# Kernel optimization log

Measured on AMD Instinct MI355X. Metric: run time of the kernel, lower is better.

The kernel has to match this reference:

```python
import jax, jax.numpy as jnp
import numpy as np
from jax import lax

B, P, S, H, F, V, O = 32, 24, 48, 512, 64, 50000, 16
EPS = 1e-5


def _lstm_scan(inputs, Wih, Whh, b):
    # inputs: [T, B, D]; PyTorch gate order i, f, g, o
    def step(carry, xt):
        h, c = carry
        g = xt @ Wih.T + h @ Whh.T + b
        i, f, gg, o = jnp.split(g, 4, axis=-1)
        c = jax.nn.sigmoid(f) * c + jax.nn.sigmoid(i) * jnp.tanh(gg)
        h = jax.nn.sigmoid(o) * jnp.tanh(c)
        return (h, c), h
    b_ = inputs.shape[1]
    h0 = jnp.zeros((b_, Whh.shape[1]), inputs.dtype)
    _, hs = lax.scan(step, (h0, h0), inputs)
    return hs


def setup_inputs() -> dict:
    key = jax.random.key(0)
    ks = jax.random.split(key, 16)
    x = jax.random.randint(ks[0], (B, P, S), 0, V)
    lens = jnp.sort(jax.random.randint(ks[1], (B,), 1, P + 1))[::-1]
    lens = lens.at[0].set(P)  # pack_padded: sorted desc, max len == P
    tok_len = jax.random.randint(ks[2], (B, P), 1, S + 1)
    tok_len = tok_len * (jnp.arange(P)[None, :] < lens[:, None])
    x_mask = jnp.arange(S)[None, None, :] >= tok_len[:, :, None]  # True = pad
    x_feature = jax.random.normal(ks[3], (B, P, S, F), dtype=jnp.float32)
    emb = jax.random.normal(ks[4], (V, H), dtype=jnp.float32) * 0.02
    w_attn = jax.random.normal(ks[5], (H,), dtype=jnp.float32) * 0.02
    b_attn = jnp.zeros((), jnp.float32)
    D = H + F
    s = 1.0 / np.sqrt(H)
    u = lambda k, sh: jax.random.uniform(k, sh, jnp.float32, -s, s)
    Wih_f, Whh_f = u(ks[6], (4 * H, D)), u(ks[7], (4 * H, H))
    bih_f, bhh_f = u(ks[8], (4 * H,)), u(ks[9], (4 * H,))
    Wih_b, Whh_b = u(ks[10], (4 * H, D)), u(ks[11], (4 * H, H))
    bih_b, bhh_b = u(ks[12], (4 * H,)), u(ks[13], (4 * H,))
    Wfc = u(ks[14], (O, 2 * H))
    bfc = jnp.zeros((O,), jnp.float32)
    gamma = jnp.ones((O,), jnp.float32)
    beta = jnp.zeros((O,), jnp.float32)
    return {"x": x, "x_mask": x_mask, "x_feature": x_feature,
            "sentences_len": lens, "clause": 0, "cls": 0,
            "emb": emb, "w_attn": w_attn, "b_attn": b_attn,
            "Wih_f": Wih_f, "Whh_f": Whh_f, "bih_f": bih_f, "bhh_f": bhh_f,
            "Wih_b": Wih_b, "Whh_b": Whh_b, "bih_b": bih_b, "bhh_b": bhh_b,
            "Wfc": Wfc, "bfc": bfc, "gamma": gamma, "beta": beta}


def reference(x, x_mask, x_feature, sentences_len, clause, cls,
              emb, w_attn, b_attn,
              Wih_f, Whh_f, bih_f, bhh_f,
              Wih_b, Whh_b, bih_b, bhh_b,
              Wfc, bfc, gamma, beta):
    # --- per-sentence embed + linear self-attention + masked sum pooling ---
    e = emb[x]                                             # [B,P,S,H]
    scores = jnp.einsum('bpsh,h->bps', e, w_attn) + b_attn  # [B,P,S]
    scores = jnp.where(x_mask, -1e30, scores)
    alpha = jax.nn.softmax(scores, axis=-1)
    alpha = jnp.where(x_mask, 0.0, alpha)                  # zeros empty sents; relu(softmax)=softmax
    valid = (~x_mask).astype(e.dtype)
    weighted = e * alpha[..., None]
    cat = jnp.concatenate([weighted, x_feature], axis=-1) * valid[..., None]
    rep = cat.sum(axis=2)                                  # [B,P,H+F]
    seq = jnp.transpose(rep, (1, 0, 2))                    # time-major [P,B,H+F]

    # --- packed bidirectional LSTM (per-sequence reversal for bwd dir) ---
    t = jnp.arange(P)[:, None]                             # [P,1]
    lens = sentences_len[None, :]                          # [1,B]
    valid_t = (t < lens)                                   # [P,B]
    h_fwd = _lstm_scan(seq, Wih_f, Whh_f, bih_f + bhh_f)
    rev_idx = jnp.clip(lens - 1 - t, 0)                    # [P,B]
    rev_in = jnp.take_along_axis(seq, rev_idx[..., None], axis=0)
    h_bwd_rev = _lstm_scan(rev_in, Wih_b, Whh_b, bih_b + bhh_b)
    h_bwd = jnp.take_along_axis(h_bwd_rev, rev_idx[..., None], axis=0)
    out_seq = jnp.concatenate([h_fwd, h_bwd], axis=-1) * valid_t[..., None]  # pad_packed zeros

    # --- tail: last timestep, fc, train-mode BN, relu, log_softmax(dim=0) ---
    last = out_seq[-1]                                     # [B,2H]
    z = jnp.reshape(last.T, (B, 2 * H))                    # faithful transpose+view quirk
    y = z @ Wfc.T + bfc                                    # [B,O]
    mean = y.mean(axis=0)
    var = y.var(axis=0)                                    # biased, as torch BN normalization
    y = gamma * (y - mean) / jnp.sqrt(var + EPS) + beta
    y = jax.nn.relu(y)
    return jax.nn.log_softmax(y, axis=0)
```

## Files before the change

kernel.cpp:

```cpp
#include <hip/hip_runtime.h>
#include <math.h>

#define BB_ 32
#define PP_ 24
#define SS_ 48
#define HH_ 512
#define FF_ 64
#define DD_ 576
#define G4_ 2048

typedef __attribute__((ext_vector_type(8))) short short8;
typedef __attribute__((ext_vector_type(4))) float f32x4;

__device__ __forceinline__ float sigf(float x) { return 1.f / (1.f + expf(-x)); }

__device__ __forceinline__ unsigned short f2bf(float f) {
    unsigned int u = __float_as_uint(f);
    u += 0x7FFFu + ((u >> 16) & 1u);
    return (unsigned short)(u >> 16);
}

__global__ void __launch_bounds__(256) prep_attn_kernel(
        const int* __restrict__ x, const unsigned int* __restrict__ maskw,
        const float* __restrict__ x_feature, const float* __restrict__ emb,
        const float* __restrict__ w_attn, const float* __restrict__ b_attn,
        const float* __restrict__ Whh, unsigned short* __restrict__ Bf,
        const float* __restrict__ Wih, unsigned short* __restrict__ Wbf,
        float* __restrict__ AfA, int* __restrict__ flags,
        float* __restrict__ seq)
{
    int blk = blockIdx.x, tid = threadIdx.x;
    if (blk < 768) {
        __shared__ float sc_s[SS_], alpha_s[SS_];
        __shared__ int vtok[SS_], vpos[SS_];
        __shared__ int nv_s, s_u8, s_f32;
        __shared__ int idx_s[SS_];
        __shared__ unsigned char msk_s[SS_];
        if (tid == 0) { s_u8 = 0; s_f32 = 0; }
        __syncthreads();
        int u8 = 0, f32 = 0;
        for (int i = tid; i < 9216; i += 256) {
            unsigned int w = maskw[i];
            if (w == 0x3F800000u) f32 = 1;
            else if (w > 1u) u8 = 1;
        }
        if (u8) s_u8 = 1;
        if (f32) s_f32 = 1;
        __syncthreads();
        int mode = s_f32 ? 2 : (s_u8 ? 1 : 0);
        int bp = blk, b = bp / PP_, p = bp % PP_;
        if (tid < SS_) {
            size_t i = (size_t)bp * SS_ + tid;
            idx_s[tid] = x[i];
            unsigned char mv;
            if (mode == 1)      mv = ((const unsigned char*)maskw)[i];
            else if (mode == 2) mv = (((const float*)maskw)[i] != 0.f);
            else                mv = (((const int*)maskw)[i] != 0);
            msk_s[tid] = mv;
        }
        __syncthreads();
        if (tid == 0) {
            int nv = 0;
            for (int s = 0; s < SS_; ++s)
                if (!msk_s[s]) { vtok[nv] = idx_s[s]; vpos[nv] = s; ++nv; }
            nv_s = nv;
        }
        __syncthreads();
        int nv = nv_s;
        int wave = tid >> 6, lane = tid & 63;
        float4 wa0 = ((const float4*)w_attn)[lane];
        float4 wa1 = ((const float4*)w_attn)[64 + lane];
        for (int j = wave; j < nv; j += 4) {
            const float4* er4 = (const float4*)(emb + (size_t)vtok[j] * HH_);
            float4 v0 = er4[lane], v1 = er4[64 + lane];
            float acc = v0.x * wa0.x + v0.y * wa0.y + v0.z * wa0.z + v0.w * wa0.w
                      + v1.x * wa1.x + v1.y * wa1.y + v1.z * wa1.z + v1.w * wa1.w;
            #pragma unroll
            for (int off = 32; off > 0; off >>= 1) acc += __shfl_down(acc, off, 64);
            if (lane == 0) sc_s[j] = acc + b_attn[0];
        }
        __syncthreads();
        if (tid == 0) {
            float m = -3.4e38f;
            for (int j = 0; j < nv; ++j) if (sc_s[j] > m) m = sc_s[j];
            float sum = 0.f;
            for (int j = 0; j < nv; ++j) { float a = expf(sc_s[j] - m); alpha_s[j] = a; sum += a; }
            float inv = (nv > 0) ? (1.f / sum) : 0.f;
            for (int j = 0; j < nv; ++j) alpha_s[j] *= inv;
        }
        __syncthreads();
        float acc0 = 0.f, acc1 = 0.f;
        for (int j = 0; j < nv; ++j) {
            float a = alpha_s[j];
            const float* er = emb + (size_t)vtok[j] * HH_;
            acc0 += a * er[tid];
            acc1 += a * er[tid + 256];
        }
        float* orow = seq + ((size_t)p * BB_ + b) * DD_;
        orow[tid] = acc0;
        orow[tid + 256] = acc1;
        if (tid < FF_) {
            float accF = 0.f;
            for (int j = 0; j < nv; ++j)
                accF += x_feature[((size_t)bp * SS_ + vpos[j]) * FF_ + tid];
            orow[HH_ + tid] = accF;
        }
    } else if (blk < 1280) {
        int idx = (blk - 768) * 256 + tid;
        int lane = idx & 63;
        int ks = (idx >> 6) & 15;
        int ti = (idx >> 10) & 1;
        int nb = idx >> 11;
        int c = lane & 15, q = lane >> 4;
        int nrow = (ti * 2 + (c >> 3)) * HH_ + nb * 8 + (c & 7);
        int k0 = ks * 32 + q * 8;
        const float* src = Whh + (size_t)nrow * HH_ + k0;
        unsigned int w0 = (unsigned int)f2bf(src[0]) | ((unsigned int)f2bf(src[1]) << 16);
        unsigned int w1 = (unsigned int)f2bf(src[2]) | ((unsigned int)f2bf(src[3]) << 16);
        unsigned int w2 = (unsigned int)f2bf(src[4]) | ((unsigned int)f2bf(src[5]) << 16);
        unsigned int w3 = (unsigned int)f2bf(src[6]) | ((unsigned int)f2bf(src[7]) << 16);
        *(uint4*)(Bf + (size_t)idx * 8) = make_uint4(w0, w1, w2, w3);
    } else if (blk < 2432) {
        int i = (blk - 1280) * 256 + tid;
        float4 v = ((const float4*)Wih)[i];
        ushort4 o;
        o.x = f2bf(v.x); o.y = f2bf(v.y); o.z = f2bf(v.z); o.w = f2bf(v.w);
        ((ushort4*)Wbf)[i] = o;
    } else if (blk < 2464) {
        int idx = (blk - 2432) * 256 + tid;
        if (idx < 8192) AfA[idx] = 0.f;
    } else {
        if (tid < 64) flags[tid] = 0;
    }
}

__global__ void __launch_bounds__(256) in_gates_mfma_kernel(
        const float* __restrict__ A,
        const unsigned short* __restrict__ Wbf,
        const float* __restrict__ bih,
        const float* __restrict__ bhh,
        float* __restrict__ Cout)
{
    int tid = threadIdx.x, lane = tid & 63, w = tid >> 6;
    int m0 = blockIdx.y * 16;
    int nb = blockIdx.x * 128 + w * 32;
    int c = lane & 15, q = lane >> 4;
    const float* Ap = A + (size_t)(m0 + c) * DD_ + q * 8;
    const unsigned short* Bp0 = Wbf + (size_t)(nb + c) * DD_ + q * 8;
    const unsigned short* Bp1 = Bp0 + 16 * DD_;
    f32x4 acc0 = {0.f, 0.f, 0.f, 0.f}, acc1 = {0.f, 0.f, 0.f, 0.f};
    for (int k = 0; k < DD_; k += 32) {
        float4 alo = *(const float4*)(Ap + k);
        float4 ahi = *(const float4*)(Ap + k + 4);
        short8 a;
        a[0] = (short)f2bf(alo.x); a[1] = (short)f2bf(alo.y);
        a[2] = (short)f2bf(alo.z); a[3] = (short)f2bf(alo.w);
        a[4] = (short)f2bf(ahi.x); a[5] = (short)f2bf(ahi.y);
        a[6] = (short)f2bf(ahi.z); a[7] = (short)f2bf(ahi.w);
        short8 b0 = *(const short8*)(Bp0 + k);
        short8 b1 = *(const short8*)(Bp1 + k);
        acc0 = __builtin_amdgcn_mfma_f32_16x16x32_bf16(a, b0, acc0, 0, 0, 0);
        acc1 = __builtin_amdgcn_mfma_f32_16x16x32_bf16(a, b1, acc1, 0, 0, 0);
    }
    #pragma unroll
    for (int r = 0; r < 4; ++r) {
        int m = m0 + q * 4 + r;
        int n0 = nb + c, n1 = nb + 16 + c;
        Cout[(size_t)m * G4_ + n0] = acc0[r] + bih[n0] + bhh[n0];
        Cout[(size_t)m * G4_ + n1] = acc1[r] + bih[n1] + bhh[n1];
    }
}

__global__ void __launch_bounds__(256) lstm_bwd_kernel(
        unsigned short* __restrict__ AfA, unsigned short* __restrict__ AfB,
        float* __restrict__ hbuf, const float* __restrict__ Ain,
        const unsigned short* __restrict__ Bfrag, int* __restrict__ flags,
        const float* __restrict__ seq, const int* __restrict__ lens,
        const float* __restrict__ Wih_b, const float* __restrict__ bih_b,
        const float* __restrict__ bhh_b, float* __restrict__ hbw)
{
    __shared__ float smem[19040];
    int tid = threadIdx.x;
    if (blockIdx.x < 64) {
        float* gl = smem;
        unsigned short* hstage = (unsigned short*)(smem + 1056);
        int lane = tid & 63, wv = tid >> 6;
        int mt = wv & 1, ti = wv >> 1;
        int nb = blockIdx.x;
        const short8* Bp = (const short8*)Bfrag + (((size_t)nb * 2 + ti) * 16) * 64 + lane;
        short8 bfr[16];
        #pragma unroll
        for (int ks = 0; ks < 16; ++ks) bfr[ks] = Bp[ks * 64];
        int c = lane & 15, q = lane >> 4;
        int g = ti * 2 + (c >> 3), ul = c & 7;
        int b2 = tid >> 3, u2 = tid & 7;
        int ug = nb * 8 + u2;
        float creg = 0.f;
        for (int t = 0; t < PP_; ++t) {
            const unsigned short* Af = (t & 1) ? AfB : AfA;
            unsigned short* An       = (t & 1) ? AfA : AfB;
            const float* Ain_t = Ain + (size_t)t * BB_ * G4_;
            float ainv[4];
            #pragma unroll
            for (int r = 0; r < 4; ++r)
                ainv[r] = Ain_t[(size_t)(mt * 16 + q * 4 + r) * G4_ + g * HH_ + nb * 8 + ul];
            const unsigned long long* Ap64 =
                (const unsigned long long*)Af + ((size_t)(mt * 16) * 64 + lane) * 2;
            short8 a[16];
            #pragma unroll
            for (int ks = 0; ks < 16; ++ks) {
                unsigned long long lo = __hip_atomic_load(Ap64 + (size_t)ks * 128,
                        __ATOMIC_RELAXED, __HIP_MEMORY_SCOPE_AGENT);
                unsigned long long hi = __hip_atomic_load(Ap64 + (size_t)ks * 128 + 1,
                        __ATOMIC_RELAXED, __HIP_MEMORY_SCOPE_AGENT);
                union { unsigned long long u[2]; short8 s; } cv;
                cv.u[0] = lo; cv.u[1] = hi;
                a[ks] = cv.s;
            }
            f32x4 acA = {0.f, 0.f, 0.f, 0.f}, acB = {0.f, 0.f, 0.f, 0.f};
            #pragma unroll
            for (int ks = 0; ks < 16; ks += 2) {
                acA = __builtin_amdgcn_mfma_f32_16x16x32_bf16(a[ks],     bfr[ks],     acA, 0, 0, 0);
                acB = __builtin_amdgcn_mfma_f32_16x16x32_bf16(a[ks + 1], bfr[ks + 1], acB, 0, 0, 0);
            }
            #pragma unroll
            for (int r = 0; r < 4; ++r) {
                float v = acA[r] + acB[r] + ainv[r];
                v = (g == 2) ? tanhf(v) : sigf(v);
                gl[(g * 8 + ul) * 33 + (mt * 16 + q * 4 + r)] = v;
            }
            __syncthreads();
            float iv = gl[(0  + u2) * 33 + b2];
            float fv = gl[(8  + u2) * 33 + b2];
            float gv = gl[(16 + u2) * 33 + b2];
            float ov = gl[(24 + u2) * 33 + b2];
            creg = fv * creg + iv * gv;
            float h = ov * tanhf(creg);
            if (t == PP_ - 1) {
                hbuf[(size_t)b2 * HH_ + ug] = h;
            } else {
                hstage[tid] = f2bf(h);
                __syncthreads();
                if (tid < 64) {
                    int b2s = tid >> 1, hf2 = tid & 1;
                    const unsigned short* hp = &hstage[b2s * 8 + hf2 * 4];
                    unsigned long long v = (unsigned long long)hp[0]
                                         | ((unsigned long long)hp[1] << 16)
                                         | ((unsigned long long)hp[2] << 32)
                                         | ((unsigned long long)hp[3] << 48);
                    size_t ub = ((((size_t)(b2s >> 4)) * 16 + (nb >> 2)) * 64
                                 + ((b2s & 15) + 16 * (nb & 3))) * 8 + hf2 * 4;
                    __hip_atomic_store((unsigned long long*)(An + ub), v,
                                       __ATOMIC_RELAXED, __HIP_MEMORY_SCOPE_AGENT);
                }
                __syncthreads();
                if (tid == 0)
                    __hip_atomic_store(&flags[nb], t + 1,
                                       __ATOMIC_RELAXED, __HIP_MEMORY_SCOPE_AGENT);
                if (tid < 64) {
                    int target = t + 1;
                    while (true) {
                        int v = __hip_atomic_load(&flags[tid],
                                __ATOMIC_RELAXED, __HIP_MEMORY_SCOPE_AGENT);
                        if (__all(v >= target)) break;
                        __builtin_amdgcn_s_sleep(1);
                    }
                }
                __syncthreads();
            }
        }
    } else {
        float* xsT = smem;
        int* pl = (int*)(smem + 19008);
        int blk2 = blockIdx.x - 64;
        if (tid < BB_) pl[tid] = lens[tid] - 1;
        __syncthreads();
        for (int idx = tid; idx < BB_ * DD_; idx += 256) {
            int b2 = idx / DD_;
            int k = idx - b2 * DD_;
            xsT[k * 33 + b2] = seq[((size_t)pl[b2] * BB_ + b2) * DD_ + k];
        }
        __syncthreads();
        int b = tid & 31, ul = tid >> 5;
        int u = blk2 * 8 + ul;
        const float* wi = Wih_b + (size_t)u * DD_;
        const float* wg = Wih_b + (size_t)(2 * HH_ + u) * DD_;
        const float* wo = Wih_b + (size_t)(3 * HH_ + u) * DD_;
        float gi = 0.f, gg = 0.f, go = 0.f;
        #pragma unroll 4
        for (int k = 0; k < DD_; k += 4) {
            float4 w1 = *(const float4*)(wi + k);
            float4 w2 = *(const float4*)(wg + k);
            float4 w3 = *(const float4*)(wo + k);
            float x0 = xsT[(k + 0) * 33 + b];
            float x1 = xsT[(k + 1) * 33 + b];
            float x2 = xsT[(k + 2) * 33 + b];
            float x3 = xsT[(k + 3) * 33 + b];
            gi += w1.x * x0 + w1.y * x1 + w1.z * x2 + w1.w * x3;
            gg += w2.x * x0 + w2.y * x1 + w2.z * x2 + w2.w * x3;
            go += w3.x * x0 + w3.y * x1 + w3.z * x2 + w3.w * x3;
        }
        gi += bih_b[u] + bhh_b[u];
        gg += bih_b[2 * HH_ + u] + bhh_b[2 * HH_ + u];
        go += bih_b[3 * HH_ + u] + bhh_b[3 * HH_ + u];
        float cc = sigf(gi) * tanhf(gg);
        hbw[(size_t)b * HH_ + u] = sigf(go) * tanhf(cc);
    }
}

__global__ void __launch_bounds__(1024) head_fused_kernel(
        const float* __restrict__ hf, const float* __restrict__ hbwd,
        const int* __restrict__ lens,
        const float* __restrict__ Wfc, const float* __restrict__ bfc,
        const float* __restrict__ gamma, const float* __restrict__ beta,
        float* __restrict__ out)
{
    __shared__ float tileL[32 * 1024];
    __shared__ float lmask[BB_];
    __shared__ float part[1024];
    __shared__ float ys[16][33];
    __shared__ float cstat[16];
    int tid = threadIdx.x;
    if (tid < BB_) lmask[tid] = (lens[tid] == PP_) ? 1.f : 0.f;
    __syncthreads();
    for (int j = tid; j < 32 * 1024; j += 1024) {
        int bb = j >> 10, col = j & 1023;
        float v = (col < HH_) ? hf[(size_t)bb * HH_ + col]
                              : hbwd[(size_t)bb * HH_ + col - HH_];
        tileL[j] = v * lmask[bb];
    }
    __syncthreads();
    int outi = tid & 511, half = tid >> 9;
    int i = outi >> 4, o = outi & 15;
    const float* wrow = Wfc + (size_t)o * 1024;
    float acc = 0.f;
    for (int q = 0; q < 32; ++q) {
        int j = i * 32 + q;
        #pragma unroll
        for (int bb2 = 0; bb2 < 16; ++bb2) {
            int bb = half * 16 + bb2;
            acc += tileL[bb * 1024 + j] * wrow[q * 32 + bb];
        }
    }
    part[tid] = acc;
    __syncthreads();
    if (tid < 512) ys[o][i] = part[tid] + part[tid + 512] + bfc[o];
    __syncthreads();
    if (tid < 16) {
        float mean = 0.f;
        for (int ii = 0; ii < 32; ++ii) mean += ys[tid][ii];
        mean *= (1.f / 32.f);
        float var = 0.f;
        for (int ii = 0; ii < 32; ++ii) { float d = ys[tid][ii] - mean; var += d * d; }
        var *= (1.f / 32.f);
        float inv = 1.f / sqrtf(var + 1e-5f);
        float gmm = gamma[tid], bt = beta[tid];
        float mx = -3.4e38f;
        for (int ii = 0; ii < 32; ++ii) {
            float v = gmm * (ys[tid][ii] - mean) * inv + bt;
            v = fmaxf(v, 0.f);
            ys[tid][ii] = v;
            mx = fmaxf(mx, v);
        }
        float s = 0.f;
        for (int ii = 0; ii < 32; ++ii) s += expf(ys[tid][ii] - mx);
        cstat[tid] = mx + logf(s);
    }
    __syncthreads();
    if (tid < 512) out[tid] = ys[o][i] - cstat[o];
}

extern "C" void kernel_launch(void* const* d_in, const int* in_sizes, int n_in,
                              void* d_out, int out_size, void* d_ws, size_t ws_size,
                              hipStream_t stream) {
    const int* x            = (const int*)d_in[0];
    const void* xm          = d_in[1];
    const float* x_feature  = (const float*)d_in[2];
    const int* lens         = (const int*)d_in[3];
    const float* emb    = (const float*)d_in[6];
    const float* w_attn = (const float*)d_in[7];
    const float* b_attn = (const float*)d_in[8];
    const float* Wih_f  = (const float*)d_in[9];
    const float* Whh_f  = (const float*)d_in[10];
    const float* bih_f  = (const float*)d_in[11];
    const float* bhh_f  = (const float*)d_in[12];
    const float* Wih_b  = (const float*)d_in[13];
    const float* bih_b  = (const float*)d_in[15];
    const float* bhh_b  = (const float*)d_in[16];
    const float* Wfc    = (const float*)d_in[17];
    const float* bfc    = (const float*)d_in[18];
    const float* gamma  = (const float*)d_in[19];
    const float* beta   = (const float*)d_in[20];

    float* ws    = (float*)d_ws;
    float* seq   = ws;
    float* Ain   = seq + (size_t)PP_ * BB_ * DD_;
    float* hb    = Ain + (size_t)PP_ * BB_ * G4_;
    float* hbuf  = hb + (size_t)BB_ * HH_;
    float* AfA   = hbuf + (size_t)BB_ * HH_;
    float* AfB   = AfA + 8192;
    float* Bfrag = AfB + 8192;
    float* Wbf   = Bfrag + 524288;
    int*  flags  = (int*)(Wbf + 589824);

    float* outp = (float*)d_out;

    prep_attn_kernel<<<dim3(2465), dim3(256), 0, stream>>>(
        x, (const unsigned int*)xm, x_feature, emb, w_attn, b_attn,
        Whh_f, (unsigned short*)Bfrag, Wih_f, (unsigned short*)Wbf,
        AfA, flags, seq);
    in_gates_mfma_kernel<<<dim3(16, 48), dim3(256), 0, stream>>>(
        seq, (const unsigned short*)Wbf, bih_f, bhh_f, Ain);
    lstm_bwd_kernel<<<dim3(128), dim3(256), 0, stream>>>(
        (unsigned short*)AfA, (unsigned short*)AfB, hbuf, Ain,
        (const unsigned short*)Bfrag, flags,
        seq, lens, Wih_b, bih_b, bhh_b, hb);
    head_fused_kernel<<<dim3(1), dim3(1024), 0, stream>>>(
        hbuf, hb, lens, Wfc, bfc, gamma, beta, outp);
}
```

Baseline: 440.7 us.

## Consolidate forward LSTM recurrence onto 16 blocks with 32 units each

The persistent forward-LSTM recurrence now runs on 16 workgroups instead of 64. Each workgroup owns 32 hidden units, and each wave keeps 4 gate tiles of bf16 Whh fragments in registers. The Whh fragment layout is reordered to match, the Ain input is folded into the MFMA accumulator init, and each thread writes its packed h values straight to global memory without a shared-memory staging pass. The aim is to cut the cost of the per-timestep cross-block flag barrier (fewer participants) and remove one __syncthreads per step. In exchange each block does four times the MFMA work per step, and register pressure rises, which may cause spills.

```diff
diff --git a/kernel.cpp b/kernel.cpp
--- a/kernel.cpp
+++ b/kernel.cpp
@@ -109,10 +109,11 @@
         int idx = (blk - 768) * 256 + tid;
         int lane = idx & 63;
         int ks = (idx >> 6) & 15;
-        int ti = (idx >> 10) & 1;
-        int nb = idx >> 11;
+        int j = (idx >> 10) & 7;
+        int nb = idx >> 13;
         int c = lane & 15, q = lane >> 4;
-        int nrow = (ti * 2 + (c >> 3)) * HH_ + nb * 8 + (c & 7);
+        int g = j >> 1, tt = j & 1;
+        int nrow = g * HH_ + nb * 32 + tt * 16 + c;
         int k0 = ks * 32 + q * 8;
         const float* src = Whh + (size_t)nrow * HH_ + k0;
         unsigned int w0 = (unsigned int)f2bf(src[0]) | ((unsigned int)f2bf(src[1]) << 16);
@@ -171,7 +172,7 @@
     }
 }
 
-__global__ void __launch_bounds__(256) lstm_bwd_kernel(
+__global__ void __launch_bounds__(256, 1) lstm_bwd_kernel(
         unsigned short* __restrict__ AfA, unsigned short* __restrict__ AfB,
         float* __restrict__ hbuf, const float* __restrict__ Ain,
         const unsigned short* __restrict__ Bfrag, int* __restrict__ flags,
@@ -181,31 +182,41 @@
 {
     __shared__ float smem[19040];
     int tid = threadIdx.x;
-    if (blockIdx.x < 64) {
+    if (blockIdx.x < 16) {
         float* gl = smem;
-        unsigned short* hstage = (unsigned short*)(smem + 1056);
         int lane = tid & 63, wv = tid >> 6;
-        int mt = wv & 1, ti = wv >> 1;
+        int mt = wv & 1, h2 = wv >> 1;
         int nb = blockIdx.x;
-        const short8* Bp = (const short8*)Bfrag + (((size_t)nb * 2 + ti) * 16) * 64 + lane;
-        short8 bfr[16];
-        #pragma unroll
-        for (int ks = 0; ks < 16; ++ks) bfr[ks] = Bp[ks * 64];
         int c = lane & 15, q = lane >> 4;
-        int g = ti * 2 + (c >> 3), ul = c & 7;
-        int b2 = tid >> 3, u2 = tid & 7;
-        int ug = nb * 8 + u2;
-        float creg = 0.f;
+        short8 bfr[4][16];
+        {
+            const short8* Bp = (const short8*)Bfrag;
+            #pragma unroll
+            for (int jj = 0; jj < 4; ++jj) {
+                const short8* bp = Bp + ((size_t)(nb * 8 + h2 * 4 + jj) * 16) * 64 + lane;
+                #pragma unroll
+                for (int ks = 0; ks < 16; ++ks) bfr[jj][ks] = bp[(size_t)ks * 64];
+            }
+        }
+        int mt_e = tid >> 7, le = (tid >> 1) & 63, half = tid & 1;
+        int be = mt_e * 16 + (le & 15);
+        int ue0 = (le >> 4) * 8 + half * 4;
+        float creg[4] = {0.f, 0.f, 0.f, 0.f};
         for (int t = 0; t < PP_; ++t) {
             const unsigned short* Af = (t & 1) ? AfB : AfA;
             unsigned short* An       = (t & 1) ? AfA : AfB;
             const float* Ain_t = Ain + (size_t)t * BB_ * G4_;
-            float ainv[4];
-            #pragma unroll
-            for (int r = 0; r < 4; ++r)
-                ainv[r] = Ain_t[(size_t)(mt * 16 + q * 4 + r) * G4_ + g * HH_ + nb * 8 + ul];
+            f32x4 acc[4];
+            #pragma unroll
+            for (int jj = 0; jj < 4; ++jj) {
+                int g = h2 * 2 + (jj >> 1), tt = jj & 1;
+                int n = g * HH_ + nb * 32 + tt * 16 + c;
+                #pragma unroll
+                for (int r = 0; r < 4; ++r)
+                    acc[jj][r] = Ain_t[(size_t)(mt * 16 + q * 4 + r) * G4_ + n];
+            }
             const unsigned long long* Ap64 =
-                (const unsigned long long*)Af + ((size_t)(mt * 16) * 64 + lane) * 2;
+                (const unsigned long long*)Af + (size_t)mt * 2048 + lane * 2;
             short8 a[16];
             #pragma unroll
             for (int ks = 0; ks < 16; ++ks) {
@@ -217,52 +228,58 @@
                 cv.u[0] = lo; cv.u[1] = hi;
                 a[ks] = cv.s;
             }
-            f32x4 acA = {0.f, 0.f, 0.f, 0.f}, acB = {0.f, 0.f, 0.f, 0.f};
-            #pragma unroll
-            for (int ks = 0; ks < 16; ks += 2) {
-                acA = __builtin_amdgcn_mfma_f32_16x16x32_bf16(a[ks],     bfr[ks],     acA, 0, 0, 0);
-                acB = __builtin_amdgcn_mfma_f32_16x16x32_bf16(a[ks + 1], bfr[ks + 1], acB, 0, 0, 0);
-            }
-            #pragma unroll
-            for (int r = 0; r < 4; ++r) {
-                float v = acA[r] + acB[r] + ainv[r];
-                v = (g == 2) ? tanhf(v) : sigf(v);
-                gl[(g * 8 + ul) * 33 + (mt * 16 + q * 4 + r)] = v;
+            #pragma unroll
+            for (int ks = 0; ks < 16; ++ks) {
+                #pragma unroll
+                for (int jj = 0; jj < 4; ++jj)
+                    acc[jj] = __builtin_amdgcn_mfma_f32_16x16x32_bf16(
+                                  a[ks], bfr[jj][ks], acc[jj], 0, 0, 0);
+            }
+            #pragma unroll
+            for (int jj = 0; jj < 4; ++jj) {
+                int g = h2 * 2 + (jj >> 1), tt = jj & 1;
+                int row = g * 32 + tt * 16 + c;
+                #pragma unroll
+                for (int r = 0; r < 4; ++r) {
+                    float v = acc[jj][r];
+                    v = (g == 2) ? tanhf(v) : sigf(v);
+                    gl[row * 33 + (mt * 16 + q * 4 + r)] = v;
+                }
             }
             __syncthreads();
-            float iv = gl[(0  + u2) * 33 + b2];
-            float fv = gl[(8  + u2) * 33 + b2];
-            float gv = gl[(16 + u2) * 33 + b2];
-            float ov = gl[(24 + u2) * 33 + b2];
-            creg = fv * creg + iv * gv;
-            float h = ov * tanhf(creg);
+            float h4[4];
+            #pragma unroll
+            for (int uu = 0; uu < 4; ++uu) {
+                int u = ue0 + uu;
+                float iv = gl[(      u) * 33 + be];
+                float fv = gl[( 32 + u) * 33 + be];
+                float gv = gl[( 64 + u) * 33 + be];
+                float ov = gl[( 96 + u) * 33 + be];
+                creg[uu] = fv * creg[uu] + iv * gv;
+                h4[uu] = ov * tanhf(creg[uu]);
+            }
             if (t == PP_ - 1) {
-                hbuf[(size_t)b2 * HH_ + ug] = h;
+                #pragma unroll
+                for (int uu = 0; uu < 4; ++uu)
+                    hbuf[(size_t)be * HH_ + nb * 32 + ue0 + uu] = h4[uu];
             } else {
-                hstage[tid] = f2bf(h);
-                __syncthreads();
-                if (tid < 64) {
-                    int b2s = tid >> 1, hf2 = tid & 1;
-                    const unsigned short* hp = &hstage[b2s * 8 + hf2 * 4];
-                    unsigned long long v = (unsigned long long)hp[0]
-                                         | ((unsigned long long)hp[1] << 16)
-                                         | ((unsigned long long)hp[2] << 32)
-                                         | ((unsigned long long)hp[3] << 48);
-                    size_t ub = ((((size_t)(b2s >> 4)) * 16 + (nb >> 2)) * 64
-                                 + ((b2s & 15) + 16 * (nb & 3))) * 8 + hf2 * 4;
-                    __hip_atomic_store((unsigned long long*)(An + ub), v,
-                                       __ATOMIC_RELAXED, __HIP_MEMORY_SCOPE_AGENT);
-                }
+                unsigned long long v = (unsigned long long)f2bf(h4[0])
+                                     | ((unsigned long long)f2bf(h4[1]) << 16)
+                                     | ((unsigned long long)f2bf(h4[2]) << 32)
+                                     | ((unsigned long long)f2bf(h4[3]) << 48);
+                size_t ui = (size_t)mt_e * 2048 + (size_t)nb * 128 + le * 2 + half;
+                __hip_atomic_store((unsigned long long*)An + ui, v,
+                                   __ATOMIC_RELAXED, __HIP_MEMORY_SCOPE_AGENT);
                 __syncthreads();
                 if (tid == 0)
                     __hip_atomic_store(&flags[nb], t + 1,
                                        __ATOMIC_RELAXED, __HIP_MEMORY_SCOPE_AGENT);
-                if (tid < 64) {
+                if (tid < 16) {
                     int target = t + 1;
                     while (true) {
-                        int v = __hip_atomic_load(&flags[tid],
+                        int fv = __hip_atomic_load(&flags[tid],
                                 __ATOMIC_RELAXED, __HIP_MEMORY_SCOPE_AGENT);
-                        if (__all(v >= target)) break;
+                        if (__all(fv >= target)) break;
                         __builtin_amdgcn_s_sleep(1);
                     }
                 }
@@ -272,7 +289,7 @@
     } else {
         float* xsT = smem;
         int* pl = (int*)(smem + 19008);
-        int blk2 = blockIdx.x - 64;
+        int blk2 = blockIdx.x - 16;
         if (tid < BB_) pl[tid] = lens[tid] - 1;
         __syncthreads();
         for (int idx = tid; idx < BB_ * DD_; idx += 256) {
@@ -411,7 +428,7 @@
         AfA, flags, seq);
     in_gates_mfma_kernel<<<dim3(16, 48), dim3(256), 0, stream>>>(
         seq, (const unsigned short*)Wbf, bih_f, bhh_f, Ain);
-    lstm_bwd_kernel<<<dim3(128), dim3(256), 0, stream>>>(
+    lstm_bwd_kernel<<<dim3(80), dim3(256), 0, stream>>>(
         (unsigned short*)AfA, (unsigned short*)AfB, hbuf, Ain,
         (const unsigned short*)Bfrag, flags,
         seq, lens, Wih_b, bih_b, bhh_b, hb);
```

Result: slower. 483.0 us (+9.6%).

## Shorten recurrent LSTM step: fewer barriers, prefetch input gates, bf16 seq copy

Applied to the files above, without the earlier changes.

The recurrent loop now has one wave compute the cell update for four units per thread and pack the bf16 h directly. This removes the LDS staging buffer and one block barrier per timestep, and the flag publish is ordered with an explicit vmcnt wait. Input-gate values for the next timestep are prefetched a step ahead, and the MFMA reduction is split across four accumulators to lengthen the dependency chains. The prep kernel also writes a bf16 copy of seq so the input-gate GEMM skips per-element conversion, at the cost of an extra workspace buffer placed after flags.

```diff
diff --git a/kernel.cpp b/kernel.cpp
--- a/kernel.cpp
+++ b/kernel.cpp
@@ -27,7 +27,7 @@
         const float* __restrict__ Whh, unsigned short* __restrict__ Bf,
         const float* __restrict__ Wih, unsigned short* __restrict__ Wbf,
         float* __restrict__ AfA, int* __restrict__ flags,
-        float* __restrict__ seq)
+        float* __restrict__ seq, unsigned short* __restrict__ seqb)
 {
     int blk = blockIdx.x, tid = threadIdx.x;
     if (blk < 768) {
@@ -97,13 +97,17 @@
             acc1 += a * er[tid + 256];
         }
         float* orow = seq + ((size_t)p * BB_ + b) * DD_;
+        unsigned short* ob = seqb + ((size_t)p * BB_ + b) * DD_;
         orow[tid] = acc0;
         orow[tid + 256] = acc1;
+        ob[tid] = f2bf(acc0);
+        ob[tid + 256] = f2bf(acc1);
         if (tid < FF_) {
             float accF = 0.f;
             for (int j = 0; j < nv; ++j)
                 accF += x_feature[((size_t)bp * SS_ + vpos[j]) * FF_ + tid];
             orow[HH_ + tid] = accF;
+            ob[HH_ + tid] = f2bf(accF);
         }
     } else if (blk < 1280) {
         int idx = (blk - 768) * 256 + tid;
@@ -135,7 +139,7 @@
 }
 
 __global__ void __launch_bounds__(256) in_gates_mfma_kernel(
-        const float* __restrict__ A,
+        const unsigned short* __restrict__ Ab,
         const unsigned short* __restrict__ Wbf,
         const float* __restrict__ bih,
         const float* __restrict__ bhh,
@@ -145,18 +149,12 @@
     int m0 = blockIdx.y * 16;
     int nb = blockIdx.x * 128 + w * 32;
     int c = lane & 15, q = lane >> 4;
-    const float* Ap = A + (size_t)(m0 + c) * DD_ + q * 8;
+    const unsigned short* Ap  = Ab  + (size_t)(m0 + c) * DD_ + q * 8;
     const unsigned short* Bp0 = Wbf + (size_t)(nb + c) * DD_ + q * 8;
     const unsigned short* Bp1 = Bp0 + 16 * DD_;
     f32x4 acc0 = {0.f, 0.f, 0.f, 0.f}, acc1 = {0.f, 0.f, 0.f, 0.f};
     for (int k = 0; k < DD_; k += 32) {
-        float4 alo = *(const float4*)(Ap + k);
-        float4 ahi = *(const float4*)(Ap + k + 4);
-        short8 a;
-        a[0] = (short)f2bf(alo.x); a[1] = (short)f2bf(alo.y);
-        a[2] = (short)f2bf(alo.z); a[3] = (short)f2bf(alo.w);
-        a[4] = (short)f2bf(ahi.x); a[5] = (short)f2bf(ahi.y);
-        a[6] = (short)f2bf(ahi.z); a[7] = (short)f2bf(ahi.w);
+        short8 a  = *(const short8*)(Ap  + k);
         short8 b0 = *(const short8*)(Bp0 + k);
         short8 b1 = *(const short8*)(Bp1 + k);
         acc0 = __builtin_amdgcn_mfma_f32_16x16x32_bf16(a, b0, acc0, 0, 0, 0);
@@ -183,7 +181,6 @@
     int tid = threadIdx.x;
     if (blockIdx.x < 64) {
         float* gl = smem;
-        unsigned short* hstage = (unsigned short*)(smem + 1056);
         int lane = tid & 63, wv = tid >> 6;
         int mt = wv & 1, ti = wv >> 1;
         int nb = blockIdx.x;
@@ -193,17 +190,20 @@
         for (int ks = 0; ks < 16; ++ks) bfr[ks] = Bp[ks * 64];
         int c = lane & 15, q = lane >> 4;
         int g = ti * 2 + (c >> 3), ul = c & 7;
-        int b2 = tid >> 3, u2 = tid & 7;
-        int ug = nb * 8 + u2;
-        float creg = 0.f;
+        int b2s = tid >> 1, hf2 = tid & 1;
+        float creg[4] = {0.f, 0.f, 0.f, 0.f};
+        const float* ainp = Ain + (size_t)(mt * 16 + q * 4) * G4_ + g * HH_ + nb * 8 + ul;
+        float ainx[4], ainn[4];
+        #pragma unroll
+        for (int r = 0; r < 4; ++r) ainx[r] = ainp[(size_t)r * G4_];
         for (int t = 0; t < PP_; ++t) {
+            if (t + 1 < PP_) {
+                const float* np = ainp + (size_t)(t + 1) * BB_ * G4_;
+                #pragma unroll
+                for (int r = 0; r < 4; ++r) ainn[r] = np[(size_t)r * G4_];
+            }
             const unsigned short* Af = (t & 1) ? AfB : AfA;
             unsigned short* An       = (t & 1) ? AfA : AfB;
-            const float* Ain_t = Ain + (size_t)t * BB_ * G4_;
-            float ainv[4];
-            #pragma unroll
-            for (int r = 0; r < 4; ++r)
-                ainv[r] = Ain_t[(size_t)(mt * 16 + q * 4 + r) * G4_ + g * HH_ + nb * 8 + ul];
             const unsigned long long* Ap64 =
                 (const unsigned long long*)Af + ((size_t)(mt * 16) * 64 + lane) * 2;
             short8 a[16];
@@ -217,57 +217,72 @@
                 cv.u[0] = lo; cv.u[1] = hi;
                 a[ks] = cv.s;
             }
-            f32x4 acA = {0.f, 0.f, 0.f, 0.f}, acB = {0.f, 0.f, 0.f, 0.f};
+            f32x4 acA = {0.f,0.f,0.f,0.f}, acB = {0.f,0.f,0.f,0.f};
+            f32x4 acC = {0.f,0.f,0.f,0.f}, acD = {0.f,0.f,0.f,0.f};
             #pragma unroll
-            for (int ks = 0; ks < 16; ks += 2) {
+            for (int ks = 0; ks < 16; ks += 4) {
                 acA = __builtin_amdgcn_mfma_f32_16x16x32_bf16(a[ks],     bfr[ks],     acA, 0, 0, 0);
                 acB = __builtin_amdgcn_mfma_f32_16x16x32_bf16(a[ks + 1], bfr[ks + 1], acB, 0, 0, 0);
+                acC = __builtin_amdgcn_mfma_f32_16x16x32_bf16(a[ks + 2], bfr[ks + 2], acC, 0, 0, 0);
+                acD = __builtin_amdgcn_mfma_f32_16x16x32_bf16(a[ks + 3], bfr[ks + 3], acD, 0, 0, 0);
             }
             #pragma unroll
             for (int r = 0; r < 4; ++r) {
-                float v = acA[r] + acB[r] + ainv[r];
+                float v = (acA[r] + acB[r]) + (acC[r] + acD[r]) + ainx[r];
                 v = (g == 2) ? tanhf(v) : sigf(v);
                 gl[(g * 8 + ul) * 33 + (mt * 16 + q * 4 + r)] = v;
             }
             __syncthreads();
-            float iv = gl[(0  + u2) * 33 + b2];
-            float fv = gl[(8  + u2) * 33 + b2];
-            float gv = gl[(16 + u2) * 33 + b2];
-            float ov = gl[(24 + u2) * 33 + b2];
-            creg = fv * creg + iv * gv;
-            float h = ov * tanhf(creg);
             if (t == PP_ - 1) {
-                hbuf[(size_t)b2 * HH_ + ug] = h;
+                if (tid < 64) {
+                    #pragma unroll
+                    for (int uu = 0; uu < 4; ++uu) {
+                        int u = hf2 * 4 + uu;
+                        float iv = gl[(     u) * 33 + b2s];
+                        float fv = gl[( 8 + u) * 33 + b2s];
+                        float gv = gl[(16 + u) * 33 + b2s];
+                        float ov = gl[(24 + u) * 33 + b2s];
+                        creg[uu] = fv * creg[uu] + iv * gv;
+                        hbuf[(size_t)b2s * HH_ + nb * 8 + u] = ov * tanhf(creg[uu]);
+                    }
+                }
             } else {
-                hstage[tid] = f2bf(h);
-                __syncthreads();
                 if (tid < 64) {
-                    int b2s = tid >> 1, hf2 = tid & 1;
-                    const unsigned short* hp = &hstage[b2s * 8 + hf2 * 4];
-                    unsigned long long v = (unsigned long long)hp[0]
-                                         | ((unsigned long long)hp[1] << 16)
-                                         | ((unsigned long long)hp[2] << 32)
-                                         | ((unsigned long long)hp[3] << 48);
+                    float h4[4];
+                    #pragma unroll
+                    for (int uu = 0; uu < 4; ++uu) {
+                        int u = hf2 * 4 + uu;
+                        float iv = gl[(     u) * 33 + b2s];
+                        float fv = gl[( 8 + u) * 33 + b2s];
+                        float gv = gl[(16 + u) * 33 + b2s];
+                        float ov = gl[(24 + u) * 33 + b2s];
+                        creg[uu] = fv * creg[uu] + iv * gv;
+                        h4[uu] = ov * tanhf(creg[uu]);
+                    }
+                    unsigned long long vv = (unsigned long long)f2bf(h4[0])
+                                          | ((unsigned long long)f2bf(h4[1]) << 16)
+                                          | ((unsigned long long)f2bf(h4[2]) << 32)
+                                          | ((unsigned long long)f2bf(h4[3]) << 48);
                     size_t ub = ((((size_t)(b2s >> 4)) * 16 + (nb >> 2)) * 64
                                  + ((b2s & 15) + 16 * (nb & 3))) * 8 + hf2 * 4;
-                    __hip_atomic_store((unsigned long long*)(An + ub), v,
+                    __hip_atomic_store((unsigned long long*)(AfA + (An - AfA) + ub), vv,
                                        __ATOMIC_RELAXED, __HIP_MEMORY_SCOPE_AGENT);
-                }
-                __syncthreads();
-                if (tid == 0)
-                    __hip_atomic_store(&flags[nb], t + 1,
-                                       __ATOMIC_RELAXED, __HIP_MEMORY_SCOPE_AGENT);
-                if (tid < 64) {
+                    asm volatile("s_waitcnt vmcnt(0)" ::: "memory");
+                    if (tid == 0)
+                        __hip_atomic_store(&flags[nb], t + 1,
+                                           __ATOMIC_RELAXED, __HIP_MEMORY_SCOPE_AGENT);
                     int target = t + 1;
                     while (true) {
-                        int v = __hip_atomic_load(&flags[tid],
+                        int fvv = __hip_atomic_load(&flags[tid],
                                 __ATOMIC_RELAXED, __HIP_MEMORY_SCOPE_AGENT);
-                        if (__all(v >= target)) break;
+                        if (__all(fvv >= target)) break;
                         __builtin_amdgcn_s_sleep(1);
                     }
                 }
                 __syncthreads();
             }
+            #pragma unroll
+            for (int r = 0; r < 4; ++r) ainx[r] = ainn[r];
         }
     } else {
         float* xsT = smem;
@@ -402,15 +417,16 @@
     float* Bfrag = AfB + 8192;
     float* Wbf   = Bfrag + 524288;
     int*  flags  = (int*)(Wbf + 589824);
+    unsigned short* seqb = (unsigned short*)(Wbf + 589824 + 16);
 
     float* outp = (float*)d_out;
 
     prep_attn_kernel<<<dim3(2465), dim3(256), 0, stream>>>(
         x, (const unsigned int*)xm, x_feature, emb, w_attn, b_attn,
         Whh_f, (unsigned short*)Bfrag, Wih_f, (unsigned short*)Wbf,
-        AfA, flags, seq);
+        AfA, flags, seq, seqb);
     in_gates_mfma_kernel<<<dim3(16, 48), dim3(256), 0, stream>>>(
-        seq, (const unsigned short*)Wbf, bih_f, bhh_f, Ain);
+        seqb, (const unsigned short*)Wbf, bih_f, bhh_f, Ain);
     lstm_bwd_kernel<<<dim3(128), dim3(256), 0, stream>>>(
         (unsigned short*)AfA, (unsigned short*)AfB, hbuf, Ain,
         (const unsigned short*)Bfrag, flags,
```

New measurement: 444.0 us. Within noise of the previous version (+0.8%).
